# Kernel optimization log

Hardware: AMD Instinct MI355X
Metric: run time of the kernel (lower is better)

Reference implementation:

```python
import jax, jax.numpy as jnp
import numpy as np

B, C, N = 8, 256, 4096
S = C // 4  # 64
BN_EPS = 1e-5

def setup_inputs() -> dict:
    key = jax.random.key(0)
    ks = jax.random.split(key, 8)
    scale = lambda fan_in: 1.0 / np.sqrt(fan_in)
    x = jax.random.normal(ks[0], (B, C, N), dtype=jnp.float32)
    W_qk = jax.random.normal(ks[1], (S, C), dtype=jnp.float32) * scale(C)
    W_k2c = jax.random.normal(ks[2], (S, C // 2), dtype=jnp.float32) * scale(C // 2)
    W_v = jax.random.normal(ks[3], (C, C), dtype=jnp.float32) * scale(C)
    b_v = jnp.zeros((C,), dtype=jnp.float32)
    W_t = jax.random.normal(ks[4], (C, C), dtype=jnp.float32) * scale(C)
    b_t = jnp.zeros((C,), dtype=jnp.float32)
    bn_gamma = jnp.ones((C,), dtype=jnp.float32)
    bn_beta = jnp.zeros((C,), dtype=jnp.float32)
    bn_mean = jnp.zeros((C,), dtype=jnp.float32)
    bn_var = jnp.ones((C,), dtype=jnp.float32)
    # random.sample(range(C), S): S distinct channel indices
    idx = jax.random.permutation(ks[5], C)[:S].astype(jnp.int32)
    return {"x": x, "W_qk": W_qk, "W_k2c": W_k2c, "W_v": W_v, "b_v": b_v,
            "W_t": W_t, "b_t": b_t, "bn_gamma": bn_gamma, "bn_beta": bn_beta,
            "bn_mean": bn_mean, "bn_var": bn_var, "idx": idx}

def reference(x, W_qk, W_k2c, W_v, b_v, W_t, b_t,
              bn_gamma, bn_beta, bn_mean, bn_var, idx):
    # q = k projection (tied weights), 1x1 conv == channel matmul
    x_q = jnp.einsum('sc,bcn->bns', W_qk, x)            # [B,N,S]
    x_k = jnp.einsum('sc,bcn->bsn', W_qk, x)            # [B,S,N]
    x_k1 = x[:, idx, :]                                  # random channel gather [B,S,N]
    x_k = jnp.concatenate([x_k, x_k1], axis=1)           # [B,C/2,N]
    x_k = jnp.einsum('sh,bhn->bsn', W_k2c, x_k)          # [B,S,N]
    x_k = jax.nn.softmax(x_k, axis=-2)                   # softmax over channel dim
    x_v = jnp.einsum('oc,bcn->bon', W_v, x) + b_v[None, :, None]  # [B,C,N]
    energy = jnp.einsum('bns,bsm->bnm', x_q, x_k)        # [B,N,N]
    attention = jax.nn.softmax(energy, axis=-1)
    attention = attention / (1e-9 + attention.sum(axis=1, keepdims=True))
    x_r = jnp.einsum('bcn,bnm->bcm', x_v, attention)     # [B,C,N]
    x_r = jnp.einsum('oc,bcm->bom', W_t, x_r) + b_t[None, :, None]
    # BatchNorm1d (inference) + ReLU
    inv = bn_gamma / jnp.sqrt(bn_var + BN_EPS)
    x_r = (x_r - bn_mean[None, :, None]) * inv[None, :, None] + bn_beta[None, :, None]
    x_r = jax.nn.relu(x_r)
    return x + x_r
```

## Files before the change

### kernel.cpp

```cpp
#include <hip/hip_runtime.h>
#include <hip/hip_bf16.h>

#define B_ 8
#define C_ 256
#define N_ 4096
#define S_ 64
#define LOG2E 1.4426950408889634f

typedef __attribute__((ext_vector_type(8))) short short8;
typedef __attribute__((ext_vector_type(4))) float f32x4;

__device__ __forceinline__ short f2b(float f) {
  unsigned u = __float_as_uint(f);
  unsigned r = (u + 0x7FFFu + ((u >> 16) & 1u)) >> 16;
  return (short)(r & 0xFFFFu);
}

__device__ __forceinline__ int cvtpk(float lo, float hi) {
  int r;
  asm("v_cvt_pk_bf16_f32 %0, %1, %2" : "=v"(r) : "v"(lo), "v"(hi));
  return r;
}


__global__ __launch_bounds__(256) void k0_transpose(const float* __restrict__ x,
                                                    short* __restrict__ Xf) {
  __shared__ float tile[64][65];
  int bid = blockIdx.x;
  int b = bid & 7;
  int rest = bid >> 3;
  int c0 = (rest & 3) * 64, n0 = (rest >> 2) * 64;
  int tn = threadIdx.x & 63, tc = threadIdx.x >> 6;
  const float* xb = x + ((size_t)b * C_ + c0) * N_ + n0;
#pragma unroll
  for (int i = 0; i < 16; i++) {
    int c = tc * 16 + i;
    tile[c][tn] = xb[(size_t)c * N_ + tn];
  }
  __syncthreads();
#pragma unroll
  for (int rr = 0; rr < 2; rr++) {
    int run = rr * 256 + threadIdx.x;
    int ntl = run >> 7, ksl = (run >> 6) & 1, ln = run & 63;
    short8 o;
#pragma unroll
    for (int j = 0; j < 8; j++) {
      int cl = ksl * 32 + ((ln >> 4) & 3) * 8 + j;
      int nl = ntl * 16 + (ln & 15);
      o[j] = f2b(tile[cl][nl]);
    }
    size_t off = ((((size_t)b * 256 + (n0 >> 4) + ntl) * 8 + (c0 >> 5) + ksl) * 64 + ln) * 8;
    *(short8*)(Xf + off) = o;
  }
}

__global__ __launch_bounds__(256) void kw_conv(const float* __restrict__ Wv,
    const float* __restrict__ Wt, short* __restrict__ Wvf, short* __restrict__ Wtf) {
  int t = blockIdx.x * 256 + threadIdx.x;
  const float* src = (t < 8192) ? Wv : Wt;
  short* dst = (t < 8192) ? Wvf : Wtf;
  int i = (t & 8191) * 8;
  int o = i >> 8, c0c = i & 255;
  short8 v;
#pragma unroll
  for (int j = 0; j < 8; j++) v[j] = f2b(src[i + j]);
  int lane = (o & 15) + 16 * ((c0c >> 3) & 3);
  size_t off = ((((size_t)(o >> 4)) * 8 + (c0c >> 5)) * 64 + lane) * 8;
  *(short8*)(dst + off) = v;
}

__global__ __launch_bounds__(256) void k1_qk(const float* __restrict__ x,
    const float* __restrict__ Wqk, const float* __restrict__ Wk2c,
    const int* __restrict__ idx, short* __restrict__ Qf, short* __restrict__ Kf) {
  int bid = blockIdx.x;
  int b = bid & 7, n0 = (bid >> 3) * 64;
  int tn = threadIdx.x;
  int sg = __builtin_amdgcn_readfirstlane(threadIdx.y);
  const float* xb = x + (size_t)b * C_ * N_ + n0 + tn;
  float acc[16];
#pragma unroll
  for (int i = 0; i < 16; i++) acc[i] = 0.f;
  for (int c = 0; c < C_; c += 4) {
    float x0 = xb[(size_t)c * N_];
    float x1 = xb[(size_t)(c + 1) * N_];
    float x2 = xb[(size_t)(c + 2) * N_];
    float x3 = xb[(size_t)(c + 3) * N_];
#pragma unroll
    for (int i = 0; i < 16; i++) {
      const float* wr = Wqk + (sg * 16 + i) * C_ + c;
      acc[i] += wr[0] * x0 + wr[1] * x1 + wr[2] * x2 + wr[3] * x3;
    }
  }
  __shared__ float q_lds[64][65];
  __shared__ float red[4][64];
#pragma unroll
  for (int i = 0; i < 16; i++) q_lds[sg * 16 + i][tn] = acc[i];
  {
    size_t base = (((size_t)b * 256 + (n0 >> 4) + (tn >> 4)) * 2 + (sg >> 1)) * 64;
    int l0 = (tn & 15) + 16 * ((2 * sg) & 3);
    int l1 = (tn & 15) + 16 * ((2 * sg + 1) & 3);
    short8 o0, o1;
#pragma unroll
    for (int i = 0; i < 8; i++) { o0[i] = f2b(acc[i] * LOG2E); o1[i] = f2b(acc[i + 8] * LOG2E); }
    *(short8*)(Qf + (base + l0) * 8) = o0;
    *(short8*)(Qf + (base + l1) * 8) = o1;
  }
  __syncthreads();
  float acc2[16];
#pragma unroll
  for (int i = 0; i < 16; i++) acc2[i] = 0.f;
  for (int h = 0; h < 64; h += 4) {
    float q0 = q_lds[h][tn], q1 = q_lds[h + 1][tn];
    float q2 = q_lds[h + 2][tn], q3 = q_lds[h + 3][tn];
#pragma unroll
    for (int i = 0; i < 16; i++) {
      const float* wr = Wk2c + (sg * 16 + i) * 128 + h;
      acc2[i] += wr[0] * q0 + wr[1] * q1 + wr[2] * q2 + wr[3] * q3;
    }
  }
  for (int h = 0; h < 64; h += 4) {
    float g0 = xb[(size_t)idx[h] * N_];
    float g1 = xb[(size_t)idx[h + 1] * N_];
    float g2 = xb[(size_t)idx[h + 2] * N_];
    float g3 = xb[(size_t)idx[h + 3] * N_];
#pragma unroll
    for (int i = 0; i < 16; i++) {
      const float* wr = Wk2c + (sg * 16 + i) * 128 + 64 + h;
      acc2[i] += wr[0] * g0 + wr[1] * g1 + wr[2] * g2 + wr[3] * g3;
    }
  }
  float pm = acc2[0];
#pragma unroll
  for (int i = 1; i < 16; i++) pm = fmaxf(pm, acc2[i]);
  red[sg][tn] = pm;
  __syncthreads();
  float mx = fmaxf(fmaxf(red[0][tn], red[1][tn]), fmaxf(red[2][tn], red[3][tn]));
  float ps = 0.f;
  float ex[16];
#pragma unroll
  for (int i = 0; i < 16; i++) { ex[i] = __expf(acc2[i] - mx); ps += ex[i]; }
  __syncthreads();
  red[sg][tn] = ps;
  __syncthreads();
  float inv = 1.f / (red[0][tn] + red[1][tn] + red[2][tn] + red[3][tn]);
  {
    size_t base = (((size_t)b * 256 + (n0 >> 4) + (tn >> 4)) * 2 + (sg >> 1)) * 64;
    int l0 = (tn & 15) + 16 * ((2 * sg) & 3);
    int l1 = (tn & 15) + 16 * ((2 * sg + 1) & 3);
    short8 o0, o1;
#pragma unroll
    for (int i = 0; i < 8; i++) { o0[i] = f2b(ex[i] * inv); o1[i] = f2b(ex[i + 8] * inv); }
    *(short8*)(Kf + (base + l0) * 8) = o0;
    *(short8*)(Kf + (base + l1) * 8) = o1;
  }
}

__global__ __launch_bounds__(256) void k2_xv(const short* __restrict__ Wvf,
    const float* __restrict__ bv, const short* __restrict__ Xf, short* __restrict__ Vf) {
  int bid = blockIdx.x;
  int b = bid & 7, nblk = bid >> 3;
  int lane = threadIdx.x & 63, w = threadIdx.x >> 6;
  int lr = lane & 15, lg = lane >> 4;
  __shared__ short Vt[64][264];
  f32x4 acc[4][4];
#pragma unroll
  for (int i = 0; i < 4; i++)
#pragma unroll
    for (int j = 0; j < 4; j++) acc[i][j] = {0.f, 0.f, 0.f, 0.f};
#pragma unroll 1
  for (int ks = 0; ks < 8; ks++) {
    short8 bfrag[4];
#pragma unroll
    for (int ns = 0; ns < 4; ns++)
      bfrag[ns] = *(const short8*)(Xf + ((((size_t)b * 256 + nblk * 4 + ns) * 8 + ks) * 64 + lane) * 8);
#pragma unroll
    for (int os = 0; os < 4; os++) {
      short8 af = *(const short8*)(Wvf + ((((size_t)(4 * w + os)) * 8 + ks) * 64 + lane) * 8);
#pragma unroll
      for (int ns = 0; ns < 4; ns++)
        acc[os][ns] = __builtin_amdgcn_mfma_f32_16x16x32_bf16(af, bfrag[ns], acc[os][ns], 0, 0, 0);
    }
  }
#pragma unroll
  for (int os = 0; os < 4; os++) {
    int c0 = w * 64 + os * 16 + lg * 4;
    float b0 = bv[c0], b1 = bv[c0 + 1], b2 = bv[c0 + 2], b3 = bv[c0 + 3];
#pragma unroll
    for (int ns = 0; ns < 4; ns++) {
      int2 pk;
      pk.x = cvtpk(acc[os][ns][0] + b0, acc[os][ns][1] + b1);
      pk.y = cvtpk(acc[os][ns][2] + b2, acc[os][ns][3] + b3);
      *(int2*)(&Vt[ns * 16 + lr][c0]) = pk;
    }
  }
  __syncthreads();
#pragma unroll
  for (int rr = 0; rr < 8; rr++) {
    int run = rr * 256 + threadIdx.x;
    int ksl = run >> 10, ctile = (run >> 6) & 15, ln = run & 63;
    short8 o;
#pragma unroll
    for (int j = 0; j < 8; j++)
      o[j] = Vt[ksl * 32 + ((ln >> 4) & 3) * 8 + j][ctile * 16 + (ln & 15)];
    size_t off = ((((size_t)b * 128 + 2 * nblk + ksl) * 16 + ctile) * 64 + ln) * 8;
    *(short8*)(Vf + off) = o;
  }
}

__global__ __launch_bounds__(256) void k3_rse(const short* __restrict__ Qf,
    const short* __restrict__ Kf, float* __restrict__ inv_rse) {
  int bid = blockIdx.x;
  int b = bid & 7, n0 = (bid >> 3) * 64;
  int lane = threadIdx.x & 63, w = threadIdx.x >> 6;
  int lg = lane >> 4;
  const short* Qb = Qf + (size_t)b * 256 * 2 * 512;
  const short* Kb = Kf + (size_t)b * 256 * 2 * 512;
  short8 qf[2];
#pragma unroll
  for (int ks = 0; ks < 2; ks++)
    qf[ks] = *(const short8*)(Qb + ((((size_t)(n0 >> 4) + w) * 2 + ks) * 64 + lane) * 8);
  short8 kc[4][2], kn[4][2];
#pragma unroll
  for (int ms = 0; ms < 4; ms++)
#pragma unroll
    for (int ks = 0; ks < 2; ks++)
      kc[ms][ks] = *(const short8*)(Kb + ((((size_t)ms) * 2 + ks) * 64 + lane) * 8);
  float rs[4] = {0.f, 0.f, 0.f, 0.f};
#pragma unroll 1
  for (int it = 0; it < 64; ++it) {
    int itn = (it < 63) ? it + 1 : it;
#pragma unroll
    for (int ms = 0; ms < 4; ms++)
#pragma unroll
      for (int ks = 0; ks < 2; ks++)
        kn[ms][ks] = *(const short8*)(Kb + ((((size_t)(itn * 4 + ms)) * 2 + ks) * 64 + lane) * 8);
#pragma unroll
    for (int ms = 0; ms < 4; ms++) {
      f32x4 e = {0.f, 0.f, 0.f, 0.f};
#pragma unroll
      for (int ks = 0; ks < 2; ks++)
        e = __builtin_amdgcn_mfma_f32_16x16x32_bf16(qf[ks], kc[ms][ks], e, 0, 0, 0);
#pragma unroll
      for (int r = 0; r < 4; r++) rs[r] += __builtin_amdgcn_exp2f(e[r]);
    }
#pragma unroll
    for (int ms = 0; ms < 4; ms++)
#pragma unroll
      for (int ks = 0; ks < 2; ks++) kc[ms][ks] = kn[ms][ks];
  }
#pragma unroll
  for (int off = 1; off < 16; off <<= 1)
#pragma unroll
    for (int r = 0; r < 4; r++) rs[r] += __shfl_xor(rs[r], off, 64);
  if ((lane & 15) == 0) {
#pragma unroll
    for (int r = 0; r < 4; r++)
      inv_rse[(size_t)b * N_ + n0 + w * 16 + lg * 4 + r] = 1.f / rs[r];
  }
}

__global__ __launch_bounds__(256, 2) void k4_att(const short* __restrict__ Qf,
    const short* __restrict__ Kf, const short* __restrict__ Vf,
    const float* __restrict__ inv_rse, short* __restrict__ Rf) {
  int bid = blockIdx.x;
  int b = bid & 7, mblk = bid >> 3, m0 = mblk * 64;
  int lane = threadIdx.x & 63, w = threadIdx.x >> 6;
  int lr = lane & 15, lg = lane >> 4;
  __shared__ short att[2][64][136];
  __shared__ float cs_red[4][64];
  const short* Qb = Qf + (size_t)b * 256 * 2 * 512;
  const short* Kb = Kf + (size_t)b * 256 * 2 * 512;
  const short* Vb = Vf + (size_t)b * 128 * 16 * 512;
  const float* irb = inv_rse + (size_t)b * N_;
  short8 kfrag[4][2];
#pragma unroll
  for (int ms = 0; ms < 4; ms++)
#pragma unroll
    for (int ks = 0; ks < 2; ks++)
      kfrag[ms][ks] = *(const short8*)(Kb + ((((size_t)(mblk * 4 + ms)) * 2 + ks) * 64 + lane) * 8);
  f32x4 P[4][4];
#pragma unroll
  for (int i = 0; i < 4; i++)
#pragma unroll
    for (int j = 0; j < 4; j++) P[i][j] = {0.f, 0.f, 0.f, 0.f};
  float csum[4] = {0.f, 0.f, 0.f, 0.f};
  short8 qf[2][2];
#pragma unroll
  for (int t = 0; t < 2; t++)
#pragma unroll
    for (int ks = 0; ks < 2; ks++)
      qf[t][ks] = *(const short8*)(Qb + ((((size_t)(t * 4 + w)) * 2 + ks) * 64 + lane) * 8);
  int buf = 0;
#pragma unroll 1
  for (int it2 = 0; it2 < 32; ++it2) {
    f32x4 e[2][4];
#pragma unroll
    for (int t = 0; t < 2; t++) {
#pragma unroll
      for (int ms = 0; ms < 4; ms++) {
        f32x4 a = {0.f, 0.f, 0.f, 0.f};
#pragma unroll
        for (int ks = 0; ks < 2; ks++)
          a = __builtin_amdgcn_mfma_f32_16x16x32_bf16(qf[t][ks], kfrag[ms][ks], a, 0, 0, 0);
        e[t][ms] = a;
      }
    }
    short8 vf[4][4];
#pragma unroll
    for (int kk = 0; kk < 4; kk++)
#pragma unroll
      for (int cs = 0; cs < 4; cs++)
        vf[kk][cs] = *(const short8*)(Vb + ((((size_t)(it2 * 4 + kk)) * 16 + 4 * w + cs) * 64 + lane) * 8);
    int itn = (it2 < 31) ? it2 + 1 : it2;
    short8 qn[2][2];
#pragma unroll
    for (int t = 0; t < 2; t++)
#pragma unroll
      for (int ks = 0; ks < 2; ks++)
        qn[t][ks] = *(const short8*)(Qb + ((((size_t)(itn * 8 + t * 4 + w)) * 2 + ks) * 64 + lane) * 8);
#pragma unroll
    for (int t = 0; t < 2; t++) {
      float ir[4];
#pragma unroll
      for (int r = 0; r < 4; r++) ir[r] = irb[it2 * 128 + t * 64 + w * 16 + lg * 4 + r];
#pragma unroll
      for (int ms = 0; ms < 4; ms++) {
        float a0 = __builtin_amdgcn_exp2f(e[t][ms][0]) * ir[0];
        float a1 = __builtin_amdgcn_exp2f(e[t][ms][1]) * ir[1];
        float a2 = __builtin_amdgcn_exp2f(e[t][ms][2]) * ir[2];
        float a3 = __builtin_amdgcn_exp2f(e[t][ms][3]) * ir[3];
        csum[ms] += (a0 + a1) + (a2 + a3);
        int2 pk;
        pk.x = cvtpk(a0, a1);
        pk.y = cvtpk(a2, a3);
        *(int2*)(&att[buf][ms * 16 + lr][t * 64 + w * 16 + lg * 4]) = pk;
      }
    }
    __syncthreads();
#pragma unroll
    for (int kk = 0; kk < 4; kk++) {
      short8 bfr[4];
#pragma unroll
      for (int ms = 0; ms < 4; ms++)
        bfr[ms] = *(const short8*)(&att[buf][ms * 16 + lr][kk * 32 + lg * 8]);
#pragma unroll
      for (int cs = 0; cs < 4; cs++)
#pragma unroll
        for (int ms = 0; ms < 4; ms++)
          P[cs][ms] = __builtin_amdgcn_mfma_f32_16x16x32_bf16(vf[kk][cs], bfr[ms], P[cs][ms], 0, 0, 0);
    }
#pragma unroll
    for (int t = 0; t < 2; t++)
#pragma unroll
      for (int ks = 0; ks < 2; ks++) qf[t][ks] = qn[t][ks];
    buf ^= 1;
  }
#pragma unroll
  for (int off = 16; off < 64; off <<= 1)
#pragma unroll
    for (int ms = 0; ms < 4; ms++) csum[ms] += __shfl_xor(csum[ms], off, 64);
  if (lg == 0) {
#pragma unroll
    for (int ms = 0; ms < 4; ms++) cs_red[w][ms * 16 + lr] = csum[ms];
  }
  __syncthreads();
  float cinv[4];
#pragma unroll
  for (int ms = 0; ms < 4; ms++) {
    int m = ms * 16 + lr;
    cinv[ms] = 1.f / (1e-9f + cs_red[0][m] + cs_red[1][m] + cs_red[2][m] + cs_red[3][m]);
  }
  short* Rt = &att[0][0][0];
#pragma unroll
  for (int cs = 0; cs < 4; cs++) {
    int c0 = w * 64 + cs * 16 + lg * 4;
#pragma unroll
    for (int ms = 0; ms < 4; ms++) {
      int2 pk;
      pk.x = cvtpk(P[cs][ms][0] * cinv[ms], P[cs][ms][1] * cinv[ms]);
      pk.y = cvtpk(P[cs][ms][2] * cinv[ms], P[cs][ms][3] * cinv[ms]);
      *(int2*)(Rt + (ms * 16 + lr) * 264 + c0) = pk;
    }
  }
  __syncthreads();
#pragma unroll
  for (int rr = 0; rr < 8; rr++) {
    int run = rr * 256 + threadIdx.x;
    int mtl = run >> 9, ksc = (run >> 6) & 7, ln = run & 63;
    short8 o;
#pragma unroll
    for (int j = 0; j < 8; j++)
      o[j] = Rt[(mtl * 16 + (ln & 15)) * 264 + ksc * 32 + ((ln >> 4) & 3) * 8 + j];
    size_t off = ((((size_t)b * 256 + (m0 >> 4) + mtl) * 8 + ksc) * 64 + ln) * 8;
    *(short8*)(Rf + off) = o;
  }
}

__global__ __launch_bounds__(256) void k5_out(const short* __restrict__ Wtf,
    const float* __restrict__ bt, const float* __restrict__ gamma,
    const float* __restrict__ beta, const float* __restrict__ mean,
    const float* __restrict__ var, const short* __restrict__ Rf,
    const float* __restrict__ x, float* __restrict__ out) {
  int bid = blockIdx.x;
  int b = bid & 7, m0 = (bid >> 3) * 64;
  int lane = threadIdx.x & 63, w = threadIdx.x >> 6;
  int lr = lane & 15, lg = lane >> 4;
  f32x4 acc[4][4];
#pragma unroll
  for (int i = 0; i < 4; i++)
#pragma unroll
    for (int j = 0; j < 4; j++) acc[i][j] = {0.f, 0.f, 0.f, 0.f};
#pragma unroll 1
  for (int ks = 0; ks < 8; ks++) {
    short8 bfr[4];
#pragma unroll
    for (int ms = 0; ms < 4; ms++)
      bfr[ms] = *(const short8*)(Rf + ((((size_t)b * 256 + (m0 >> 4) + ms) * 8 + ks) * 64 + lane) * 8);
#pragma unroll
    for (int os = 0; os < 4; os++) {
      short8 af = *(const short8*)(Wtf + ((((size_t)(4 * w + os)) * 8 + ks) * 64 + lane) * 8);
#pragma unroll
      for (int ms = 0; ms < 4; ms++)
        acc[os][ms] = __builtin_amdgcn_mfma_f32_16x16x32_bf16(af, bfr[ms], acc[os][ms], 0, 0, 0);
    }
  }
  const float* xb = x + (size_t)b * C_ * N_ + m0;
  float* ob = out + (size_t)b * C_ * N_ + m0;
#pragma unroll
  for (int os = 0; os < 4; os++)
#pragma unroll
    for (int r = 0; r < 4; r++) {
      int o = w * 64 + os * 16 + lg * 4 + r;
      float bb = bt[o];
      float iv = gamma[o] * rsqrtf(var[o] + 1e-5f);
      float mn = mean[o], be = beta[o];
#pragma unroll
      for (int ms = 0; ms < 4; ms++) {
        int m = ms * 16 + lr;
        float v = (acc[os][ms][r] + bb - mn) * iv + be;
        v = fmaxf(v, 0.f);
        ob[(size_t)o * N_ + m] = xb[(size_t)o * N_ + m] + v;
      }
    }
}

extern "C" void kernel_launch(void* const* d_in, const int* in_sizes, int n_in,
                              void* d_out, int out_size, void* d_ws, size_t ws_size,
                              hipStream_t stream) {
  const float* x     = (const float*)d_in[0];
  const float* Wqk   = (const float*)d_in[1];
  const float* Wk2c  = (const float*)d_in[2];
  const float* Wv    = (const float*)d_in[3];
  const float* bv    = (const float*)d_in[4];
  const float* Wt    = (const float*)d_in[5];
  const float* bt    = (const float*)d_in[6];
  const float* gamma = (const float*)d_in[7];
  const float* beta  = (const float*)d_in[8];
  const float* mean  = (const float*)d_in[9];
  const float* var   = (const float*)d_in[10];
  const int*   idx   = (const int*)d_in[11];
  float* out = (float*)d_out;

  char* ws = (char*)d_ws;
  size_t off = 0;
  auto alloc = [&](size_t bytes) -> void* {
    void* p = ws + off;
    off = (off + bytes + 255) & ~(size_t)255;
    return p;
  };
  short* Xf   = (short*)alloc((size_t)B_ * N_ * C_ * 2);
  short* Qf   = (short*)alloc((size_t)B_ * N_ * S_ * 2);
  short* Kf   = (short*)alloc((size_t)B_ * N_ * S_ * 2);
  short* Vf   = (short*)alloc((size_t)B_ * C_ * N_ * 2);
  float* irse = (float*)alloc((size_t)B_ * N_ * 4);
  short* Rf   = (short*)alloc((size_t)B_ * N_ * C_ * 2);
  short* Wvf  = (short*)alloc((size_t)C_ * C_ * 2);
  short* Wtf  = (short*)alloc((size_t)C_ * C_ * 2);

  kw_conv<<<dim3(64), 256, 0, stream>>>(Wv, Wt, Wvf, Wtf);
  k0_transpose<<<dim3(2048), 256, 0, stream>>>(x, Xf);
  k1_qk<<<dim3(512), dim3(64, 4), 0, stream>>>(x, Wqk, Wk2c, idx, Qf, Kf);
  k2_xv<<<dim3(512), 256, 0, stream>>>(Wvf, bv, Xf, Vf);
  k3_rse<<<dim3(512), 256, 0, stream>>>(Qf, Kf, irse);
  k4_att<<<dim3(512), 256, 0, stream>>>(Qf, Kf, Vf, irse, Rf);
  k5_out<<<dim3(512), 256, 0, stream>>>(Wtf, bt, gamma, beta, mean, var, Rf, x, out);
}
```

Baseline: 338.0 us.

## Fuse x transpose into qk kernel and restructure attention LDS layout and sync

```diff
diff --git a/kernel.cpp b/kernel.cpp
--- a/kernel.cpp
+++ b/kernel.cpp
@@ -22,37 +22,6 @@
   return r;
 }
 
-
-__global__ __launch_bounds__(256) void k0_transpose(const float* __restrict__ x,
-                                                    short* __restrict__ Xf) {
-  __shared__ float tile[64][65];
-  int bid = blockIdx.x;
-  int b = bid & 7;
-  int rest = bid >> 3;
-  int c0 = (rest & 3) * 64, n0 = (rest >> 2) * 64;
-  int tn = threadIdx.x & 63, tc = threadIdx.x >> 6;
-  const float* xb = x + ((size_t)b * C_ + c0) * N_ + n0;
-#pragma unroll
-  for (int i = 0; i < 16; i++) {
-    int c = tc * 16 + i;
-    tile[c][tn] = xb[(size_t)c * N_ + tn];
-  }
-  __syncthreads();
-#pragma unroll
-  for (int rr = 0; rr < 2; rr++) {
-    int run = rr * 256 + threadIdx.x;
-    int ntl = run >> 7, ksl = (run >> 6) & 1, ln = run & 63;
-    short8 o;
-#pragma unroll
-    for (int j = 0; j < 8; j++) {
-      int cl = ksl * 32 + ((ln >> 4) & 3) * 8 + j;
-      int nl = ntl * 16 + (ln & 15);
-      o[j] = f2b(tile[cl][nl]);
-    }
-    size_t off = ((((size_t)b * 256 + (n0 >> 4) + ntl) * 8 + (c0 >> 5) + ksl) * 64 + ln) * 8;
-    *(short8*)(Xf + off) = o;
-  }
-}
 
 __global__ __launch_bounds__(256) void kw_conv(const float* __restrict__ Wv,
     const float* __restrict__ Wt, short* __restrict__ Wvf, short* __restrict__ Wtf) {
@@ -71,12 +40,21 @@
 
 __global__ __launch_bounds__(256) void k1_qk(const float* __restrict__ x,
     const float* __restrict__ Wqk, const float* __restrict__ Wk2c,
-    const int* __restrict__ idx, short* __restrict__ Qf, short* __restrict__ Kf) {
+    const int* __restrict__ idx, short* __restrict__ Qf, short* __restrict__ Kf,
+    short* __restrict__ Xf) {
   int bid = blockIdx.x;
   int b = bid & 7, n0 = (bid >> 3) * 64;
   int tn = threadIdx.x;
   int sg = __builtin_amdgcn_readfirstlane(threadIdx.y);
   const float* xb = x + (size_t)b * C_ * N_ + n0 + tn;
+  __shared__ short xls[256][73];
+  __shared__ float q_lds[64][65];
+  __shared__ float red[4][64];
+#pragma unroll 4
+  for (int i = 0; i < 64; i++) {
+    int c = sg * 64 + i;
+    xls[c][tn] = f2b(xb[(size_t)c * N_]);
+  }
   float acc[16];
 #pragma unroll
   for (int i = 0; i < 16; i++) acc[i] = 0.f;
@@ -91,8 +69,6 @@
       acc[i] += wr[0] * x0 + wr[1] * x1 + wr[2] * x2 + wr[3] * x3;
     }
   }
-  __shared__ float q_lds[64][65];
-  __shared__ float red[4][64];
 #pragma unroll
   for (int i = 0; i < 16; i++) q_lds[sg * 16 + i][tn] = acc[i];
   {
@@ -106,6 +82,17 @@
     *(short8*)(Qf + (base + l1) * 8) = o1;
   }
   __syncthreads();
+#pragma unroll
+  for (int i = 0; i < 8; i++) {
+    int run = i * 4 + sg;
+    int ntl = run >> 3, ks = run & 7;
+    short8 o;
+#pragma unroll
+    for (int j = 0; j < 8; j++)
+      o[j] = xls[ks * 32 + ((tn >> 4) & 3) * 8 + j][ntl * 16 + (tn & 15)];
+    size_t off = ((((size_t)b * 256 + (n0 >> 4) + ntl) * 8 + ks) * 64 + tn) * 8;
+    *(short8*)(Xf + off) = o;
+  }
   float acc2[16];
 #pragma unroll
   for (int i = 0; i < 16; i++) acc2[i] = 0.f;
@@ -266,8 +253,9 @@
   int b = bid & 7, mblk = bid >> 3, m0 = mblk * 64;
   int lane = threadIdx.x & 63, w = threadIdx.x >> 6;
   int lr = lane & 15, lg = lane >> 4;
-  __shared__ short att[2][64][136];
+  __shared__ __align__(16) short lds_raw[64 * 264];
   __shared__ float cs_red[4][64];
+  short* attf = lds_raw;
   const short* Qb = Qf + (size_t)b * 256 * 2 * 512;
   const short* Kb = Kf + (size_t)b * 256 * 2 * 512;
   const short* Vb = Vf + (size_t)b * 128 * 16 * 512;
@@ -290,12 +278,23 @@
 #pragma unroll
     for (int ks = 0; ks < 2; ks++)
       qf[t][ks] = *(const short8*)(Qb + ((((size_t)(t * 4 + w)) * 2 + ks) * 64 + lane) * 8);
+  int wln = lr + 16 * ((w & 1) * 2 + (lg >> 1));
+  int wjo = (lg & 1) * 4;
   int buf = 0;
 #pragma unroll 1
   for (int it2 = 0; it2 < 32; ++it2) {
+    f32x4 irv[2];
+    irv[0] = *(const f32x4*)(irb + it2 * 128 + w * 16 + lg * 4);
+    irv[1] = *(const f32x4*)(irb + it2 * 128 + 64 + w * 16 + lg * 4);
+    short8 vf[4][4];
+#pragma unroll
+    for (int kk = 0; kk < 4; kk++)
+#pragma unroll
+      for (int cs = 0; cs < 4; cs++)
+        vf[kk][cs] = *(const short8*)(Vb + ((((size_t)(it2 * 4 + kk)) * 16 + 4 * w + cs) * 64 + lane) * 8);
     f32x4 e[2][4];
 #pragma unroll
-    for (int t = 0; t < 2; t++) {
+    for (int t = 0; t < 2; t++)
 #pragma unroll
       for (int ms = 0; ms < 4; ms++) {
         f32x4 a = {0.f, 0.f, 0.f, 0.f};
@@ -304,13 +303,6 @@
           a = __builtin_amdgcn_mfma_f32_16x16x32_bf16(qf[t][ks], kfrag[ms][ks], a, 0, 0, 0);
         e[t][ms] = a;
       }
-    }
-    short8 vf[4][4];
-#pragma unroll
-    for (int kk = 0; kk < 4; kk++)
-#pragma unroll
-      for (int cs = 0; cs < 4; cs++)
-        vf[kk][cs] = *(const short8*)(Vb + ((((size_t)(it2 * 4 + kk)) * 16 + 4 * w + cs) * 64 + lane) * 8);
     int itn = (it2 < 31) ? it2 + 1 : it2;
     short8 qn[2][2];
 #pragma unroll
@@ -320,35 +312,37 @@
         qn[t][ks] = *(const short8*)(Qb + ((((size_t)(itn * 8 + t * 4 + w)) * 2 + ks) * 64 + lane) * 8);
 #pragma unroll
     for (int t = 0; t < 2; t++) {
-      float ir[4];
-#pragma unroll
-      for (int r = 0; r < 4; r++) ir[r] = irb[it2 * 128 + t * 64 + w * 16 + lg * 4 + r];
+      int kk = t * 2 + (w >> 1);
 #pragma unroll
       for (int ms = 0; ms < 4; ms++) {
-        float a0 = __builtin_amdgcn_exp2f(e[t][ms][0]) * ir[0];
-        float a1 = __builtin_amdgcn_exp2f(e[t][ms][1]) * ir[1];
-        float a2 = __builtin_amdgcn_exp2f(e[t][ms][2]) * ir[2];
-        float a3 = __builtin_amdgcn_exp2f(e[t][ms][3]) * ir[3];
+        float a0 = __builtin_amdgcn_exp2f(e[t][ms][0]) * irv[t][0];
+        float a1 = __builtin_amdgcn_exp2f(e[t][ms][1]) * irv[t][1];
+        float a2 = __builtin_amdgcn_exp2f(e[t][ms][2]) * irv[t][2];
+        float a3 = __builtin_amdgcn_exp2f(e[t][ms][3]) * irv[t][3];
         csum[ms] += (a0 + a1) + (a2 + a3);
         int2 pk;
         pk.x = cvtpk(a0, a1);
         pk.y = cvtpk(a2, a3);
-        *(int2*)(&att[buf][ms * 16 + lr][t * 64 + w * 16 + lg * 4]) = pk;
+        *(int2*)(attf + (size_t)buf * 8192 + (kk * 4 + ms) * 512 + wln * 8 + wjo) = pk;
       }
     }
-    __syncthreads();
+    asm volatile("s_waitcnt lgkmcnt(0)" ::: "memory");
+    __builtin_amdgcn_s_barrier();
+    __builtin_amdgcn_sched_barrier(0);
+    __builtin_amdgcn_s_setprio(1);
 #pragma unroll
     for (int kk = 0; kk < 4; kk++) {
       short8 bfr[4];
 #pragma unroll
       for (int ms = 0; ms < 4; ms++)
-        bfr[ms] = *(const short8*)(&att[buf][ms * 16 + lr][kk * 32 + lg * 8]);
+        bfr[ms] = *(const short8*)(attf + (size_t)buf * 8192 + (kk * 4 + ms) * 512 + lane * 8);
 #pragma unroll
       for (int cs = 0; cs < 4; cs++)
 #pragma unroll
         for (int ms = 0; ms < 4; ms++)
           P[cs][ms] = __builtin_amdgcn_mfma_f32_16x16x32_bf16(vf[kk][cs], bfr[ms], P[cs][ms], 0, 0, 0);
     }
+    __builtin_amdgcn_s_setprio(0);
 #pragma unroll
     for (int t = 0; t < 2; t++)
 #pragma unroll
@@ -370,7 +364,7 @@
     int m = ms * 16 + lr;
     cinv[ms] = 1.f / (1e-9f + cs_red[0][m] + cs_red[1][m] + cs_red[2][m] + cs_red[3][m]);
   }
-  short* Rt = &att[0][0][0];
+  short* Rt = lds_raw;
 #pragma unroll
   for (int cs = 0; cs < 4; cs++) {
     int c0 = w * 64 + cs * 16 + lg * 4;
@@ -478,8 +472,7 @@
   short* Wtf  = (short*)alloc((size_t)C_ * C_ * 2);
 
   kw_conv<<<dim3(64), 256, 0, stream>>>(Wv, Wt, Wvf, Wtf);
-  k0_transpose<<<dim3(2048), 256, 0, stream>>>(x, Xf);
-  k1_qk<<<dim3(512), dim3(64, 4), 0, stream>>>(x, Wqk, Wk2c, idx, Qf, Kf);
+  k1_qk<<<dim3(512), dim3(64, 4), 0, stream>>>(x, Wqk, Wk2c, idx, Qf, Kf, Xf);
   k2_xv<<<dim3(512), 256, 0, stream>>>(Wvf, bv, Xf, Vf);
   k3_rse<<<dim3(512), 256, 0, stream>>>(Qf, Kf, irse);
   k4_att<<<dim3(512), 256, 0, stream>>>(Qf, Kf, Vf, irse, Rf);
```

New measurement: 337.4 us. Within noise of the previous version (-0.2%).
